# Optimization experiments

Hardware: AMD Instinct MI355X
Metric: run time of the kernel (lower is better)

## Reference

```python
import jax, jax.numpy as jnp
import numpy as np

N, E, F_IN, H, C, N_CLS = 50000, 800000, 128, 4, 32, 10
NEG_SLOPE = 0.2


def setup_inputs() -> dict:
    key = jax.random.key(0)
    ks = jax.random.split(key, 24)
    d = {}
    d["x"] = jax.random.normal(ks[0], (N, F_IN), jnp.float32)
    d["edge_index"] = jax.random.randint(ks[1], (2, E), 0, N, jnp.int32)

    def lin(k, fan_in, shape):
        return jax.random.normal(k, shape, jnp.float32) / np.float32(np.sqrt(fan_in))

    # conv1: F_IN -> H*C, heads H, concat
    d["W1"]  = lin(ks[2], F_IN, (F_IN, H * C))
    d["a1s"] = lin(ks[3], C, (H, C))
    d["a1d"] = lin(ks[4], C, (H, C))
    d["b1"]  = jnp.zeros((H * C,), jnp.float32)
    d["lin1_W"] = lin(ks[5], F_IN, (F_IN, H * C))
    d["lin1_b"] = jnp.zeros((H * C,), jnp.float32)
    # conv2: H*C -> H*C
    d["W2"]  = lin(ks[6], H * C, (H * C, H * C))
    d["a2s"] = lin(ks[7], C, (H, C))
    d["a2d"] = lin(ks[8], C, (H, C))
    d["b2"]  = jnp.zeros((H * C,), jnp.float32)
    d["lin2_W"] = lin(ks[9], H * C, (H * C, H * C))
    d["lin2_b"] = jnp.zeros((H * C,), jnp.float32)
    # conv3: H*C -> N_CLS, heads H, concat=False (mean over heads)
    d["W3"]  = lin(ks[10], H * C, (H * C, H * N_CLS))
    d["a3s"] = lin(ks[11], N_CLS, (H, N_CLS))
    d["a3d"] = lin(ks[12], N_CLS, (H, N_CLS))
    d["b3"]  = jnp.zeros((N_CLS,), jnp.float32)
    d["lin3_W"] = lin(ks[13], H * C, (H * C, N_CLS))
    d["lin3_b"] = jnp.zeros((N_CLS,), jnp.float32)
    return d


def gat_conv(x, src, dst, W, a_s, a_d, b, heads, out_ch, concat):
    n = x.shape[0]
    h = (x @ W).reshape(n, heads, out_ch)                # [N,H,C]
    alpha_src = jnp.sum(h * a_s, axis=-1)                # [N,H]
    alpha_dst = jnp.sum(h * a_d, axis=-1)                # [N,H]
    e = jax.nn.leaky_relu(alpha_src[src] + alpha_dst[dst], NEG_SLOPE)  # [E,H]
    # segment softmax over edges grouped by destination node
    m = jax.ops.segment_max(e, dst, num_segments=n)      # [N,H]
    p = jnp.exp(e - m[dst])
    denom = jax.ops.segment_sum(p, dst, num_segments=n)  # [N,H]
    alpha = p / (denom[dst] + 1e-16)                     # [E,H]
    out = jax.ops.segment_sum(alpha[:, :, None] * h[src], dst, num_segments=n)  # [N,H,C]
    out = out.reshape(n, heads * out_ch) if concat else out.mean(axis=1)
    return out + b


def reference(x, edge_index, W1, a1s, a1d, b1, lin1_W, lin1_b,
              W2, a2s, a2d, b2, lin2_W, lin2_b,
              W3, a3s, a3d, b3, lin3_W, lin3_b):
    n = x.shape[0]
    # PyG GATConv adds self-loops by default
    loops = jnp.arange(n, dtype=edge_index.dtype)
    src = jnp.concatenate([edge_index[0], loops])
    dst = jnp.concatenate([edge_index[1], loops])

    x = jax.nn.elu(gat_conv(x, src, dst, W1, a1s, a1d, b1, H, C, True) + x @ lin1_W + lin1_b)
    x = jax.nn.elu(gat_conv(x, src, dst, W2, a2s, a2d, b2, H, C, True) + x @ lin2_W + lin2_b)
    x = gat_conv(x, src, dst, W3, a3s, a3d, b3, H, N_CLS, False) + x @ lin3_W + lin3_b
    return x
```

## Files before the change

### kernel.cpp

```cpp
#include <hip/hip_runtime.h>
#include <math.h>


#define HEADS 4

typedef __attribute__((ext_vector_type(8))) short short8v;
typedef __attribute__((ext_vector_type(4))) float float4v;

__device__ __forceinline__ float lrelu(float v) { return v > 0.f ? v : 0.2f * v; }

__device__ __forceinline__ unsigned short f2bf(float f) {
    unsigned u = __float_as_uint(f);
    unsigned r = u + 0x7FFFu + ((u >> 16) & 1u);
    return (unsigned short)(r >> 16);
}
__device__ __forceinline__ float bf2f(unsigned short u) {
    return __uint_as_float(((unsigned)u) << 16);
}

__global__ void castX(const float* __restrict__ x, unsigned short* __restrict__ xb, int n4) {
    int i = blockIdx.x * blockDim.x + threadIdx.x;
    if (i >= n4) return;
    float4 v = *(const float4*)&x[(size_t)i * 4];
    ushort4 o;
    o.x = f2bf(v.x); o.y = f2bf(v.y); o.z = f2bf(v.z); o.w = f2bf(v.w);
    *(ushort4*)&xb[(size_t)i * 4] = o;
}

__global__ void packB12(const float* __restrict__ W, const float* __restrict__ LW,
                        const float* __restrict__ a_s, const float* __restrict__ a_d,
                        unsigned short* __restrict__ BT) {
    int i = blockIdx.x * blockDim.x + threadIdx.x;
    if (i >= 320 * 128) return;
    int m = i >> 7, k = i & 127;
    float v = 0.f;
    if (m < 128) {
        v = W[(size_t)k * 128 + m];
    } else if (m < 256) {
        v = LW[(size_t)k * 128 + (m - 128)];
    } else if (m < 260) {
        int h = m - 256;
        for (int c = 0; c < 32; ++c)
            v = fmaf(W[(size_t)k * 128 + h * 32 + c], a_s[h * 32 + c], v);
    } else if (m < 264) {
        int h = m - 260;
        for (int c = 0; c < 32; ++c)
            v = fmaf(W[(size_t)k * 128 + h * 32 + c], a_d[h * 32 + c], v);
    }
    BT[i] = f2bf(v);
}

__global__ void packB3(const float* __restrict__ W3, const float* __restrict__ LW3,
                       const float* __restrict__ a_s, const float* __restrict__ a_d,
                       unsigned short* __restrict__ BT) {
    int i = blockIdx.x * blockDim.x + threadIdx.x;
    if (i >= 128 * 128) return;
    int m = i >> 7, k = i & 127;
    float v = 0.f;
    if (m < 40) {
        v = W3[(size_t)k * 40 + m];
    } else if (m < 50) {
        v = LW3[(size_t)k * 10 + (m - 40)];
    } else if (m >= 64 && m < 68) {
        int h = m - 64;
        for (int c = 0; c < 10; ++c)
            v = fmaf(W3[(size_t)k * 40 + h * 10 + c], a_s[h * 10 + c], v);
    } else if (m >= 68 && m < 72) {
        int h = m - 68;
        for (int c = 0; c < 10; ++c)
            v = fmaf(W3[(size_t)k * 40 + h * 10 + c], a_d[h * 10 + c], v);
    }
    BT[i] = f2bf(v);
}

__global__ __launch_bounds__(256) void mfma_gemm(const unsigned short* __restrict__ A,
                                                 const unsigned short* __restrict__ BT,
                                                 unsigned short* __restrict__ C,
                                                 float* __restrict__ asrc,
                                                 float* __restrict__ adst,
                                                 int nrows, int Mc, int Cstride,
                                                 int permStore) {
    const int wave = threadIdx.x >> 6;
    const int lane = threadIdx.x & 63;
    const int row0 = blockIdx.y * 64 + wave * 16;
    const int col0 = blockIdx.x * 64;
    const int lrow = lane & 15;
    const int kgrp = lane >> 4;
    const bool alphaBlk = (col0 >= Mc);

    float4v acc[4] = {{0.f,0.f,0.f,0.f},{0.f,0.f,0.f,0.f},{0.f,0.f,0.f,0.f},{0.f,0.f,0.f,0.f}};

    int arow = row0 + lrow;
    if (arow >= nrows) arow = nrows - 1;
    const unsigned short* Ap = A + (size_t)arow * 128 + kgrp * 8;
    const unsigned short* Bp = BT + (size_t)(col0 + lrow) * 128 + kgrp * 8;

    if (alphaBlk) {
#pragma unroll
        for (int t = 0; t < 4; ++t) {
            short8v a  = *(const short8v*)(Ap + t * 32);
            short8v b0 = *(const short8v*)(Bp + t * 32);
            acc[0] = __builtin_amdgcn_mfma_f32_16x16x32_bf16(a, b0, acc[0], 0, 0, 0);
        }
        if (lrow < 8) {
            float* dst = (lrow < 4) ? asrc : adst;
            int hh = lrow & 3;
#pragma unroll
            for (int r = 0; r < 4; ++r) {
                int row = row0 + kgrp * 4 + r;
                if (row < nrows) dst[(size_t)row * 4 + hh] = acc[0][r];
            }
        }
        return;
    }

#pragma unroll
    for (int t = 0; t < 4; ++t) {
        short8v a = *(const short8v*)(Ap + t * 32);
#pragma unroll
        for (int kk = 0; kk < 4; ++kk) {
            short8v b = *(const short8v*)(Bp + kk * 16 * 128 + t * 32);
            acc[kk] = __builtin_amdgcn_mfma_f32_16x16x32_bf16(a, b, acc[kk], 0, 0, 0);
        }
    }

#pragma unroll
    for (int r = 0; r < 4; ++r) {
        int row = row0 + kgrp * 4 + r;
        if (row >= nrows) continue;
        if (!permStore) {
            size_t base = (size_t)row * Cstride + col0 + lrow;
            C[base]      = f2bf(acc[0][r]);
            C[base + 16] = f2bf(acc[1][r]);
            C[base + 32] = f2bf(acc[2][r]);
            C[base + 48] = f2bf(acc[3][r]);
        } else {
#pragma unroll
            for (int kk = 0; kk < 4; ++kk) {
                int col = lrow + kk * 16;
                int pos;
                if (col < 40)      pos = (col / 5) * 8 + (col % 5);
                else if (col < 50) pos = 64 + (col - 40);
                else continue;
                C[(size_t)row * 80 + pos] = f2bf(acc[kk][r]);
            }
        }
    }
}

__global__ void deg_hist4(const int* __restrict__ dst, int E, int* __restrict__ deg) {
    int e = (blockIdx.x * blockDim.x + threadIdx.x) * 4;
    if (e + 3 < E) {
        int4 d = *(const int4*)&dst[e];
        atomicAdd(&deg[d.x], 1);
        atomicAdd(&deg[d.y], 1);
        atomicAdd(&deg[d.z], 1);
        atomicAdd(&deg[d.w], 1);
    } else {
        for (; e < E; ++e) atomicAdd(&deg[dst[e]], 1);
    }
}

__global__ void scan_block(const int* __restrict__ in, int* __restrict__ out,
                           int* __restrict__ bsum, int n) {
    __shared__ int tmp[256];
    int i = blockIdx.x * 256 + threadIdx.x;
    int v = (i < n) ? in[i] + 1 : 0;
    tmp[threadIdx.x] = v;
    __syncthreads();
    for (int d = 1; d < 256; d <<= 1) {
        int t = (threadIdx.x >= d) ? tmp[threadIdx.x - d] : 0;
        __syncthreads();
        tmp[threadIdx.x] += t;
        __syncthreads();
    }
    if (i < n) out[i] = tmp[threadIdx.x] - v;
    if (threadIdx.x == 255) bsum[blockIdx.x] = tmp[255];
}

__global__ void scan_bsum(int* bsum, int nb) {
    __shared__ int tmp[256];
    int v = (threadIdx.x < nb) ? bsum[threadIdx.x] : 0;
    tmp[threadIdx.x] = v;
    __syncthreads();
    for (int d = 1; d < 256; d <<= 1) {
        int t = (threadIdx.x >= d) ? tmp[threadIdx.x - d] : 0;
        __syncthreads();
        tmp[threadIdx.x] += t;
        __syncthreads();
    }
    if (threadIdx.x < nb) bsum[threadIdx.x] = tmp[threadIdx.x] - v;
}

__global__ void scan_add(int* out, const int* __restrict__ bsum, int n) {
    int i = blockIdx.x * 256 + threadIdx.x;
    if (i < n) out[i] += bsum[blockIdx.x];
}

#define FILL_U 4
__global__ __launch_bounds__(256) void csr_fill_bucket(
    const int* __restrict__ ei, int E, int N,
    const int* __restrict__ rowptr, int* __restrict__ cur,
    int* __restrict__ adj)
{
    const int bucket = blockIdx.x & 7;
    const int grp    = blockIdx.x >> 3;
    const int ngrp   = gridDim.x >> 3;
    const int npb    = (N + 7) >> 3;
    const int lo = bucket * npb;
    const int hi = (lo + npb < N) ? lo + npb : N;

    for (int i = lo + grp * 256 + (int)threadIdx.x; i < hi; i += ngrp * 256)
        adj[rowptr[i]] = i;

    const int chunkSz = 256 * FILL_U;
    const int nchunks = (E + chunkSz - 1) / chunkSz;
    const int* dstRow = ei + E;
    for (int c = grp; c < nchunks; c += ngrp) {
        int base = c * chunkSz + (int)threadIdx.x;
#pragma unroll
        for (int k = 0; k < FILL_U; ++k) {
            int e = base + k * 256;
            if (e < E) {
                int d = dstRow[e];
                if (d >= lo && d < hi) {
                    int pos = rowptr[d] + 1 + atomicAdd(&cur[d], 1);
                    adj[pos] = ei[e];
                }
            }
        }
    }
}

__global__ __launch_bounds__(256) void gat_gather128(
    const int* __restrict__ rowptr, const int* __restrict__ adj, int ET,
    const float* __restrict__ asrc, const float* __restrict__ adst,
    const unsigned short* __restrict__ Hb,
    const float* __restrict__ bias, const float* __restrict__ lbias,
    unsigned short* __restrict__ xout, int n)
{
    int node = (blockIdx.x * 256 + threadIdx.x) >> 6;
    int lane = threadIdx.x & 63;
    if (node >= n) return;
    int beg = rowptr[node];
    int end = (node + 1 < n) ? rowptr[node + 1] : ET;

    int ep = lane >> 4;
    int q  = lane & 15;
    int c0 = q * 8;
    int h  = q >> 2;
    float adh = adst[(size_t)node * 4 + h];

    float accp = 0.f;
    float a[8];
#pragma unroll
    for (int k = 0; k < 8; ++k) a[k] = 0.f;

    int j = beg + ep;
    while (j < end) {
        int jb = j + 4;
        bool vb = jb < end;
        int s0 = adj[j];
        int s1 = vb ? adj[jb] : s0;
        float av0 = asrc[(size_t)s0 * 4 + h];
        float av1 = asrc[(size_t)s1 * 4 + h];
        short8v hv0 = *(const short8v*)&Hb[(size_t)s0 * 256 + c0];
        short8v hv1 = *(const short8v*)&Hb[(size_t)s1 * 256 + c0];
        float p0 = __expf(lrelu(av0 + adh));
        float p1 = vb ? __expf(lrelu(av1 + adh)) : 0.f;
        accp += p0 + p1;
#pragma unroll
        for (int k = 0; k < 8; ++k) {
            a[k] = fmaf(p0, bf2f((unsigned short)hv0[k]), a[k]);
            a[k] = fmaf(p1, bf2f((unsigned short)hv1[k]), a[k]);
        }
        j += 8;
    }
#pragma unroll
    for (int off = 16; off <= 32; off <<= 1) {
        accp += __shfl_xor(accp, off);
#pragma unroll
        for (int k = 0; k < 8; ++k) a[k] += __shfl_xor(a[k], off);
    }

    if (ep == 0) {
        float inv = 1.f / (accp + 1e-16f);
        short8v lv = *(const short8v*)&Hb[(size_t)node * 256 + 128 + c0];
        unsigned short w[8];
#pragma unroll
        for (int k = 0; k < 8; ++k) {
            float v = a[k] * inv + bias[c0 + k] + bf2f((unsigned short)lv[k]) + lbias[c0 + k];
            v = v > 0.f ? v : __expf(v) - 1.f;
            w[k] = f2bf(v);
        }
        *(short8v*)&xout[(size_t)node * 128 + c0] = *(short8v*)w;
    }
}

__global__ __launch_bounds__(256) void gat_gather40(
    const int* __restrict__ rowptr, const int* __restrict__ adj, int ET,
    const float* __restrict__ asrc, const float* __restrict__ adst,
    const unsigned short* __restrict__ Hb3,
    const float* __restrict__ bias, const float* __restrict__ lbias,
    float* __restrict__ out, int n)
{
    int node = (blockIdx.x * 256 + threadIdx.x) >> 6;
    int lane = threadIdx.x & 63;
    if (node >= n) return;
    int beg = rowptr[node];
    int end = (node + 1 < n) ? rowptr[node + 1] : ET;

    int slot = lane >> 3;
    int sub  = lane & 7;
    int h    = sub >> 1;
    float adh = adst[(size_t)node * 4 + h];

    float accp = 0.f;
    float a[5];
#pragma unroll
    for (int k = 0; k < 5; ++k) a[k] = 0.f;

    int j = beg + slot;
    bool valid = j < end;
    int sN = 0; float avN = 0.f;
    if (valid) { sN = adj[j]; avN = asrc[(size_t)sN * 4 + h]; }
    while (valid) {
        int s = sN; float av = avN;
        int j2 = j + 8;
        bool v2 = j2 < end;
        if (v2) { sN = adj[j2]; avN = asrc[(size_t)sN * 4 + h]; }
        float p = __expf(lrelu(av + adh));
        short8v hv = *(const short8v*)&Hb3[(size_t)s * 80 + sub * 8];
        accp += p;
#pragma unroll
        for (int k = 0; k < 5; ++k)
            a[k] = fmaf(p, bf2f((unsigned short)hv[k]), a[k]);
        j = j2; valid = v2;
    }
#pragma unroll
    for (int off = 8; off <= 32; off <<= 1) {
        accp += __shfl_xor(accp, off);
#pragma unroll
        for (int k = 0; k < 5; ++k) a[k] += __shfl_xor(a[k], off);
    }
    float inv = 0.25f / (accp + 1e-16f);
#pragma unroll
    for (int k = 0; k < 5; ++k) a[k] *= inv;
#pragma unroll
    for (int off = 2; off <= 4; off <<= 1) {
#pragma unroll
        for (int k = 0; k < 5; ++k) a[k] += __shfl_xor(a[k], off);
    }

    if (lane < 2) {
        int cc0 = sub * 5;
#pragma unroll
        for (int k = 0; k < 5; ++k) {
            float lin = bf2f(Hb3[(size_t)node * 80 + 64 + cc0 + k]);
            out[(size_t)node * 10 + cc0 + k] = a[k] + bias[cc0 + k] + lin + lbias[cc0 + k];
        }
    }
}

extern "C" void kernel_launch(void* const* d_in, const int* in_sizes, int n_in,
                              void* d_out, int out_size, void* d_ws, size_t ws_size,
                              hipStream_t stream) {
    const float* x   = (const float*)d_in[0];
    const int*   ei  = (const int*)d_in[1];
    const float* W1  = (const float*)d_in[2];
    const float* a1s = (const float*)d_in[3];
    const float* a1d = (const float*)d_in[4];
    const float* b1  = (const float*)d_in[5];
    const float* l1W = (const float*)d_in[6];
    const float* l1b = (const float*)d_in[7];
    const float* W2  = (const float*)d_in[8];
    const float* a2s = (const float*)d_in[9];
    const float* a2d = (const float*)d_in[10];
    const float* b2  = (const float*)d_in[11];
    const float* l2W = (const float*)d_in[12];
    const float* l2b = (const float*)d_in[13];
    const float* W3  = (const float*)d_in[14];
    const float* a3s = (const float*)d_in[15];
    const float* a3d = (const float*)d_in[16];
    const float* b3  = (const float*)d_in[17];
    const float* l3W = (const float*)d_in[18];
    const float* l3b = (const float*)d_in[19];

    const int N  = in_sizes[0] / 128;
    const int E  = in_sizes[1] / 2;
    const int ET = E + N;

    unsigned short* Xb = (unsigned short*)d_ws;
    unsigned short* Hb = Xb + (size_t)N * 128;
    unsigned short* BT = Hb + (size_t)N * 256;
    float* asrc = (float*)(BT + 320 * 128);
    float* adst = asrc + (size_t)N * 4;
    int* deg    = (int*)(adst + (size_t)N * 4);
    int* cur    = deg + N;
    int* rowptr = cur + N;
    int* bsum   = rowptr + N;
    int* adj    = bsum + 256;

    const int nScanBlocks = (N + 255) / 256;
    int waveBlocks = (N * 64 + 255) / 256;
    int rowBlocks  = (N + 63) / 64;

    hipMemsetAsync(deg, 0, (size_t)N * 2 * 4, stream);
    deg_hist4<<<(E / 4 + 256) / 256, 256, 0, stream>>>(ei + E, E, deg);
    scan_block<<<nScanBlocks, 256, 0, stream>>>(deg, rowptr, bsum, N);
    scan_bsum<<<1, 256, 0, stream>>>(bsum, nScanBlocks);
    scan_add<<<nScanBlocks, 256, 0, stream>>>(rowptr, bsum, N);
    csr_fill_bucket<<<4096, 256, 0, stream>>>(ei, E, N, rowptr, cur, adj);

    castX<<<(N * 32 + 255) / 256, 256, 0, stream>>>(x, Xb, N * 32);

    packB12<<<(320 * 128 + 255) / 256, 256, 0, stream>>>(W1, l1W, a1s, a1d, BT);
    mfma_gemm<<<dim3(5, rowBlocks), 256, 0, stream>>>(Xb, BT, Hb, asrc, adst, N, 256, 256, 0);
    gat_gather128<<<waveBlocks, 256, 0, stream>>>(rowptr, adj, ET, asrc, adst, Hb, b1, l1b, Xb, N);

    packB12<<<(320 * 128 + 255) / 256, 256, 0, stream>>>(W2, l2W, a2s, a2d, BT);
    mfma_gemm<<<dim3(5, rowBlocks), 256, 0, stream>>>(Xb, BT, Hb, asrc, adst, N, 256, 256, 0);
    gat_gather128<<<waveBlocks, 256, 0, stream>>>(rowptr, adj, ET, asrc, adst, Hb, b2, l2b, Xb, N);

    packB3<<<(128 * 128 + 255) / 256, 256, 0, stream>>>(W3, l3W, a3s, a3d, BT);
    mfma_gemm<<<dim3(2, rowBlocks), 256, 0, stream>>>(Xb, BT, Hb, asrc, adst, N, 64, 80, 1);
    gat_gather40<<<waveBlocks, 256, 0, stream>>>(rowptr, adj, ET, asrc, adst, Hb, b3, l3b, (float*)d_out, N);
}
```

Before: 311.8 us.

## Loop column blocks inside GEMM and unroll gather edge loops deeper

The MFMA GEMM now launches one block per 64-row tile and loops over all column blocks plus the alpha block. The A fragments are loaded once into registers and reused across every column tile, which cuts redundant A reads and launch width but lowers grid parallelism. The 128-wide gather now processes four edges per iteration instead of two to expose more memory-level parallelism. The 40-wide gather replaces its software-prefetch loop with a two-edge unrolled loop. The deeper unrolling raises register pressure.

```diff
diff --git a/kernel.cpp b/kernel.cpp
--- a/kernel.cpp
+++ b/kernel.cpp
@@ -82,25 +82,61 @@
                                                  int permStore) {
     const int wave = threadIdx.x >> 6;
     const int lane = threadIdx.x & 63;
-    const int row0 = blockIdx.y * 64 + wave * 16;
-    const int col0 = blockIdx.x * 64;
+    const int row0 = blockIdx.x * 64 + wave * 16;
     const int lrow = lane & 15;
     const int kgrp = lane >> 4;
-    const bool alphaBlk = (col0 >= Mc);
-
-    float4v acc[4] = {{0.f,0.f,0.f,0.f},{0.f,0.f,0.f,0.f},{0.f,0.f,0.f,0.f},{0.f,0.f,0.f,0.f}};
 
     int arow = row0 + lrow;
     if (arow >= nrows) arow = nrows - 1;
     const unsigned short* Ap = A + (size_t)arow * 128 + kgrp * 8;
-    const unsigned short* Bp = BT + (size_t)(col0 + lrow) * 128 + kgrp * 8;
-
-    if (alphaBlk) {
+
+    short8v afrag[4];
+#pragma unroll
+    for (int t = 0; t < 4; ++t) afrag[t] = *(const short8v*)(Ap + t * 32);
+
+    const int nDataBlk = Mc >> 6;
+    for (int cb = 0; cb < nDataBlk; ++cb) {
+        const unsigned short* Bp = BT + (size_t)(cb * 64 + lrow) * 128 + kgrp * 8;
+        float4v acc[4] = {{0.f,0.f,0.f,0.f},{0.f,0.f,0.f,0.f},{0.f,0.f,0.f,0.f},{0.f,0.f,0.f,0.f}};
 #pragma unroll
         for (int t = 0; t < 4; ++t) {
-            short8v a  = *(const short8v*)(Ap + t * 32);
-            short8v b0 = *(const short8v*)(Bp + t * 32);
-            acc[0] = __builtin_amdgcn_mfma_f32_16x16x32_bf16(a, b0, acc[0], 0, 0, 0);
+#pragma unroll
+            for (int kk = 0; kk < 4; ++kk) {
+                short8v b = *(const short8v*)(Bp + kk * 16 * 128 + t * 32);
+                acc[kk] = __builtin_amdgcn_mfma_f32_16x16x32_bf16(afrag[t], b, acc[kk], 0, 0, 0);
+            }
+        }
+#pragma unroll
+        for (int r = 0; r < 4; ++r) {
+            int row = row0 + kgrp * 4 + r;
+            if (row >= nrows) continue;
+            if (!permStore) {
+                size_t base = (size_t)row * Cstride + cb * 64 + lrow;
+                C[base]      = f2bf(acc[0][r]);
+                C[base + 16] = f2bf(acc[1][r]);
+                C[base + 32] = f2bf(acc[2][r]);
+                C[base + 48] = f2bf(acc[3][r]);
+            } else {
+#pragma unroll
+                for (int kk = 0; kk < 4; ++kk) {
+                    int col = lrow + kk * 16;
+                    int pos;
+                    if (col < 40)      pos = (col / 5) * 8 + (col % 5);
+                    else if (col < 50) pos = 64 + (col - 40);
+                    else continue;
+                    C[(size_t)row * 80 + pos] = f2bf(acc[kk][r]);
+                }
+            }
+        }
+    }
+
+    {
+        const unsigned short* Bp = BT + (size_t)(Mc + lrow) * 128 + kgrp * 8;
+        float4v acc0 = {0.f, 0.f, 0.f, 0.f};
+#pragma unroll
+        for (int t = 0; t < 4; ++t) {
+            short8v b = *(const short8v*)(Bp + t * 32);
+            acc0 = __builtin_amdgcn_mfma_f32_16x16x32_bf16(afrag[t], b, acc0, 0, 0, 0);
         }
         if (lrow < 8) {
             float* dst = (lrow < 4) ? asrc : adst;
@@ -108,41 +144,7 @@
 #pragma unroll
             for (int r = 0; r < 4; ++r) {
                 int row = row0 + kgrp * 4 + r;
-                if (row < nrows) dst[(size_t)row * 4 + hh] = acc[0][r];
-            }
-        }
-        return;
-    }
-
-#pragma unroll
-    for (int t = 0; t < 4; ++t) {
-        short8v a = *(const short8v*)(Ap + t * 32);
-#pragma unroll
-        for (int kk = 0; kk < 4; ++kk) {
-            short8v b = *(const short8v*)(Bp + kk * 16 * 128 + t * 32);
-            acc[kk] = __builtin_amdgcn_mfma_f32_16x16x32_bf16(a, b, acc[kk], 0, 0, 0);
-        }
-    }
-
-#pragma unroll
-    for (int r = 0; r < 4; ++r) {
-        int row = row0 + kgrp * 4 + r;
-        if (row >= nrows) continue;
-        if (!permStore) {
-            size_t base = (size_t)row * Cstride + col0 + lrow;
-            C[base]      = f2bf(acc[0][r]);
-            C[base + 16] = f2bf(acc[1][r]);
-            C[base + 32] = f2bf(acc[2][r]);
-            C[base + 48] = f2bf(acc[3][r]);
-        } else {
-#pragma unroll
-            for (int kk = 0; kk < 4; ++kk) {
-                int col = lrow + kk * 16;
-                int pos;
-                if (col < 40)      pos = (col / 5) * 8 + (col % 5);
-                else if (col < 50) pos = 64 + (col - 40);
-                else continue;
-                C[(size_t)row * 80 + pos] = f2bf(acc[kk][r]);
+                if (row < nrows) dst[(size_t)row * 4 + hh] = acc0[r];
             }
         }
     }
@@ -258,23 +260,33 @@
 
     int j = beg + ep;
     while (j < end) {
-        int jb = j + 4;
-        bool vb = jb < end;
+        int j1 = j + 4, j2 = j + 8, j3 = j + 12;
+        bool v1 = j1 < end, v2 = j2 < end, v3 = j3 < end;
         int s0 = adj[j];
-        int s1 = vb ? adj[jb] : s0;
+        int s1 = v1 ? adj[j1] : s0;
+        int s2 = v2 ? adj[j2] : s0;
+        int s3 = v3 ? adj[j3] : s0;
         float av0 = asrc[(size_t)s0 * 4 + h];
         float av1 = asrc[(size_t)s1 * 4 + h];
+        float av2 = asrc[(size_t)s2 * 4 + h];
+        float av3 = asrc[(size_t)s3 * 4 + h];
         short8v hv0 = *(const short8v*)&Hb[(size_t)s0 * 256 + c0];
         short8v hv1 = *(const short8v*)&Hb[(size_t)s1 * 256 + c0];
+        short8v hv2 = *(const short8v*)&Hb[(size_t)s2 * 256 + c0];
+        short8v hv3 = *(const short8v*)&Hb[(size_t)s3 * 256 + c0];
         float p0 = __expf(lrelu(av0 + adh));
-        float p1 = vb ? __expf(lrelu(av1 + adh)) : 0.f;
-        accp += p0 + p1;
+        float p1 = v1 ? __expf(lrelu(av1 + adh)) : 0.f;
+        float p2 = v2 ? __expf(lrelu(av2 + adh)) : 0.f;
+        float p3 = v3 ? __expf(lrelu(av3 + adh)) : 0.f;
+        accp += (p0 + p1) + (p2 + p3);
 #pragma unroll
         for (int k = 0; k < 8; ++k) {
-            a[k] = fmaf(p0, bf2f((unsigned short)hv0[k]), a[k]);
-            a[k] = fmaf(p1, bf2f((unsigned short)hv1[k]), a[k]);
-        }
-        j += 8;
+            float t0 = fmaf(p0, bf2f((unsigned short)hv0[k]), a[k]);
+            float t1 = fmaf(p1, bf2f((unsigned short)hv1[k]), t0);
+            float t2 = fmaf(p2, bf2f((unsigned short)hv2[k]), t1);
+            a[k] = fmaf(p3, bf2f((unsigned short)hv3[k]), t2);
+        }
+        j += 16;
     }
 #pragma unroll
     for (int off = 16; off <= 32; off <<= 1) {
@@ -321,21 +333,24 @@
     for (int k = 0; k < 5; ++k) a[k] = 0.f;
 
     int j = beg + slot;
-    bool valid = j < end;
-    int sN = 0; float avN = 0.f;
-    if (valid) { sN = adj[j]; avN = asrc[(size_t)sN * 4 + h]; }
-    while (valid) {
-        int s = sN; float av = avN;
-        int j2 = j + 8;
-        bool v2 = j2 < end;
-        if (v2) { sN = adj[j2]; avN = asrc[(size_t)sN * 4 + h]; }
-        float p = __expf(lrelu(av + adh));
-        short8v hv = *(const short8v*)&Hb3[(size_t)s * 80 + sub * 8];
-        accp += p;
-#pragma unroll
-        for (int k = 0; k < 5; ++k)
-            a[k] = fmaf(p, bf2f((unsigned short)hv[k]), a[k]);
-        j = j2; valid = v2;
+    while (j < end) {
+        int j1 = j + 8;
+        bool v1 = j1 < end;
+        int s0 = adj[j];
+        int s1 = v1 ? adj[j1] : s0;
+        float av0 = asrc[(size_t)s0 * 4 + h];
+        float av1 = asrc[(size_t)s1 * 4 + h];
+        short8v hv0 = *(const short8v*)&Hb3[(size_t)s0 * 80 + sub * 8];
+        short8v hv1 = *(const short8v*)&Hb3[(size_t)s1 * 80 + sub * 8];
+        float p0 = __expf(lrelu(av0 + adh));
+        float p1 = v1 ? __expf(lrelu(av1 + adh)) : 0.f;
+        accp += p0 + p1;
+#pragma unroll
+        for (int k = 0; k < 5; ++k) {
+            float t = fmaf(p0, bf2f((unsigned short)hv0[k]), a[k]);
+            a[k] = fmaf(p1, bf2f((unsigned short)hv1[k]), t);
+        }
+        j += 16;
     }
 #pragma unroll
     for (int off = 8; off <= 32; off <<= 1) {
@@ -415,14 +430,14 @@
     castX<<<(N * 32 + 255) / 256, 256, 0, stream>>>(x, Xb, N * 32);
 
     packB12<<<(320 * 128 + 255) / 256, 256, 0, stream>>>(W1, l1W, a1s, a1d, BT);
-    mfma_gemm<<<dim3(5, rowBlocks), 256, 0, stream>>>(Xb, BT, Hb, asrc, adst, N, 256, 256, 0);
+    mfma_gemm<<<rowBlocks, 256, 0, stream>>>(Xb, BT, Hb, asrc, adst, N, 256, 256, 0);
     gat_gather128<<<waveBlocks, 256, 0, stream>>>(rowptr, adj, ET, asrc, adst, Hb, b1, l1b, Xb, N);
 
     packB12<<<(320 * 128 + 255) / 256, 256, 0, stream>>>(W2, l2W, a2s, a2d, BT);
-    mfma_gemm<<<dim3(5, rowBlocks), 256, 0, stream>>>(Xb, BT, Hb, asrc, adst, N, 256, 256, 0);
+    mfma_gemm<<<rowBlocks, 256, 0, stream>>>(Xb, BT, Hb, asrc, adst, N, 256, 256, 0);
     gat_gather128<<<waveBlocks, 256, 0, stream>>>(rowptr, adj, ET, asrc, adst, Hb, b2, l2b, Xb, N);
 
     packB3<<<(128 * 128 + 255) / 256, 256, 0, stream>>>(W3, l3W, a3s, a3d, BT);
-    mfma_gemm<<<dim3(2, rowBlocks), 256, 0, stream>>>(Xb, BT, Hb, asrc, adst, N, 64, 80, 1);
+    mfma_gemm<<<rowBlocks, 256, 0, stream>>>(Xb, BT, Hb, asrc, adst, N, 64, 80, 1);
     gat_gather40<<<waveBlocks, 256, 0, stream>>>(rowptr, adj, ET, asrc, adst, Hb, b3, l3b, (float*)d_out, N);
 }
```

New measurement: 302.8 us. 1.03x faster.
